# Optimization experiments

Measured on AMD Instinct MI355X. Metric: run time of the kernel, lower is better.

## Reference

```python
import jax, jax.numpy as jnp
import numpy as np
from jax import lax

D_MODEL = 64
D_STATE = 16
D_CONV = 3
EXPAND = 2
D_INNER = EXPAND * D_MODEL  # 128
DT_RANK = (D_MODEL + 15) // 16  # 4
B, H, W = 2, 64, 64


def setup_inputs() -> dict:
    key = jax.random.key(0)
    ks = jax.random.split(key, 8)
    def n(k, shape, s=0.02):
        return jax.random.normal(k, shape, dtype=jnp.float32) * s
    return {
        "x": jax.random.normal(ks[0], (B, D_MODEL, H, W), dtype=jnp.float32),
        "ln_w": jnp.ones((D_MODEL,), jnp.float32),
        "ln_b": jnp.zeros((D_MODEL,), jnp.float32),
        "W_in": n(ks[1], (4, 2 * D_INNER, D_MODEL)),          # in_proj per direction
        "conv_w": n(ks[2], (4, D_INNER, 1, D_CONV), 0.1),     # depthwise causal conv
        "conv_b": jnp.zeros((4, D_INNER), jnp.float32),
        "W_xproj": n(ks[3], (4, DT_RANK + 2 * D_STATE, D_INNER)),
        "W_dt": n(ks[4], (4, D_INNER, DT_RANK), 0.1),
        "b_dt": n(ks[5], (4, D_INNER), 0.1),
        "A_log": jnp.log(jnp.broadcast_to(jnp.arange(1, D_STATE + 1, dtype=jnp.float32), (4, D_INNER, D_STATE))),
        "D_param": jnp.ones((4, D_INNER), jnp.float32),
        "W_out": n(ks[6], (4, D_MODEL, D_INNER)),
    }


def _mamba(x, W_in, conv_w, conv_b, W_xproj, W_dt, b_dt, A_log, Dp, W_out):
    # x: (B, L, D) -> (B, L, D). Standard Mamba forward with selective scan.
    xz = x @ W_in.T                              # (B, L, 2*d_inner)
    xp, z = jnp.split(xz, 2, axis=-1)
    xc = jnp.swapaxes(xp, 1, 2)                  # (B, d_inner, L)
    xc = lax.conv_general_dilated(xc, conv_w, (1,), [(D_CONV - 1, 0)], feature_group_count=D_INNER)
    xc = xc + conv_b[None, :, None]
    xp = jax.nn.silu(jnp.swapaxes(xc, 1, 2))     # (B, L, d_inner)
    dbl = xp @ W_xproj.T                         # (B, L, dt_rank + 2*d_state)
    dt = dbl[..., :DT_RANK]
    Bc = dbl[..., DT_RANK:DT_RANK + D_STATE]
    Cc = dbl[..., DT_RANK + D_STATE:]
    dt = jax.nn.softplus(dt @ W_dt.T + b_dt)     # (B, L, d_inner)
    A = -jnp.exp(A_log)                          # (d_inner, d_state)
    dA = jnp.exp(dt[..., None] * A)              # (B, L, d_inner, d_state)
    dBu = (dt * xp)[..., None] * Bc[:, :, None, :]

    def comb(c1, c2):
        a1, b1 = c1
        a2, b2 = c2
        return a1 * a2, a2 * b1 + b2

    _, h = lax.associative_scan(comb, (dA, dBu), axis=1)  # parallel linear recurrence
    y = jnp.einsum('blds,bls->bld', h, Cc) + xp * Dp
    y = y * jax.nn.silu(z)
    return y @ W_out.T


def reference(x, ln_w, ln_b, W_in, conv_w, conv_b, W_xproj, W_dt, b_dt, A_log, D_param, W_out):
    Bq, C, Hh, Ww = x.shape
    xn = jnp.transpose(x, (0, 2, 3, 1))          # (B, H, W, C)
    mu = xn.mean(-1, keepdims=True)
    var = xn.var(-1, keepdims=True)
    xn = (xn - mu) * lax.rsqrt(var + 1e-5) * ln_w + ln_b
    x_f = xn.reshape(Bq, Hh * Ww, C)                              # row-major scan
    x_tf = jnp.transpose(xn, (0, 2, 1, 3)).reshape(Bq, Ww * Hh, C)  # column-major scan
    xs = jnp.stack([x_f, x_f[:, ::-1], x_tf, x_tf[:, ::-1]])      # (4, B, L, C)
    ys = jax.vmap(_mamba)(xs, W_in, conv_w, conv_b, W_xproj, W_dt, b_dt, A_log, D_param, W_out)
    y = ys[0].reshape(Bq, Hh, Ww, C) + ys[1][:, ::-1].reshape(Bq, Hh, Ww, C)
    yt = ys[2].reshape(Bq, Ww, Hh, C) + ys[3][:, ::-1].reshape(Bq, Ww, Hh, C)
    y = y + jnp.transpose(yt, (0, 2, 1, 3))
    return jnp.transpose(y, (0, 3, 1, 2))        # back to (B, C, H, W)
```

## Files before the change

kernel.cpp:

```cpp
#include <hip/hip_runtime.h>
#include <math.h>


#define PP  8
#define LL  4096
#define DD  128
#define CH  16
#define NCH 256
#define LOG2E 1.4426950408889634f
#define EXP2F(x) __builtin_exp2f(x)

__device__ __forceinline__ float sigmoidf_(float x){ return 1.0f/(1.0f+__expf(-x)); }

__device__ __forceinline__ int dirmap(int dir, int t) {
  if (dir == 0) return t;
  if (dir == 1) return 4095 - t;
  int tt = (dir == 2) ? t : 4095 - t;
  return ((tt & 63) << 6) | (tt >> 6);
}

__global__ __launch_bounds__(256) void k_ln(const float* __restrict__ x,
    const float* __restrict__ lw, const float* __restrict__ lb, float* __restrict__ xn) {
  int tid = threadIdx.x;
  int lane = tid & 63;
  int pos = blockIdx.x*4 + (tid>>6);
  int b = pos >> 12, hw = pos & 4095;
  float v = x[((long)(b*64 + lane))*4096 + hw];
  float s = v;
  for (int m = 32; m; m >>= 1) s += __shfl_xor(s, m);
  float mu = s * (1.0f/64.0f);
  float dv = (v-mu)*(v-mu);
  for (int m = 32; m; m >>= 1) dv += __shfl_xor(dv, m);
  float rs = rsqrtf(dv*(1.0f/64.0f) + 1e-5f);
  xn[(long)pos*64 + lane] = (v-mu)*rs*lw[lane] + lb[lane];
}

__global__ __launch_bounds__(256) void k_gemm1(const float* __restrict__ xn,
    const float* __restrict__ Win, float* __restrict__ xz) {
  __shared__ float Ast[64][68];
  __shared__ float Bst[64][68];
  int p = blockIdx.z, dir = p >> 1, b = p & 1;
  int tid = threadIdx.x;
  int tx = tid & 15, ty = tid >> 4;
  int m0 = blockIdx.x*64, n0 = blockIdx.y*64;
  int kk4 = tid & 15, rr = tid >> 4;
  #pragma unroll
  for (int pass = 0; pass < 4; ++pass) {
    int r = pass*16 + rr;
    int l = dirmap(dir, m0 + r);
    float4 av = *(const float4*)(xn + ((long)(b*4096 + l))*64 + kk4*4);
    Ast[kk4*4+0][r]=av.x; Ast[kk4*4+1][r]=av.y; Ast[kk4*4+2][r]=av.z; Ast[kk4*4+3][r]=av.w;
    float4 bv = *(const float4*)(Win + ((long)(dir*256 + n0 + r))*64 + kk4*4);
    Bst[kk4*4+0][r]=bv.x; Bst[kk4*4+1][r]=bv.y; Bst[kk4*4+2][r]=bv.z; Bst[kk4*4+3][r]=bv.w;
  }
  __syncthreads();
  float acc[4][4] = {};
  #pragma unroll 8
  for (int kk = 0; kk < 64; ++kk) {
    float4 a = *(const float4*)(&Ast[kk][ty*4]);
    float4 bq = *(const float4*)(&Bst[kk][tx*4]);
    acc[0][0] += a.x*bq.x; acc[0][1] += a.x*bq.y; acc[0][2] += a.x*bq.z; acc[0][3] += a.x*bq.w;
    acc[1][0] += a.y*bq.x; acc[1][1] += a.y*bq.y; acc[1][2] += a.y*bq.z; acc[1][3] += a.y*bq.w;
    acc[2][0] += a.z*bq.x; acc[2][1] += a.z*bq.y; acc[2][2] += a.z*bq.z; acc[2][3] += a.z*bq.w;
    acc[3][0] += a.w*bq.x; acc[3][1] += a.w*bq.y; acc[3][2] += a.w*bq.z; acc[3][3] += a.w*bq.w;
  }
  float* Cp = xz + (long)p*4096*256;
  #pragma unroll
  for (int i = 0; i < 4; ++i)
    #pragma unroll
    for (int j = 0; j < 4; ++j)
      Cp[(long)(m0 + ty*4 + i)*256 + n0 + tx*4 + j] = acc[i][j];
}

__global__ __launch_bounds__(256) void k_gemm(const float* __restrict__ A, const float* __restrict__ Bw,
    float* __restrict__ C, int M, int N, int K, long aStr, long bStr, long cStr) {
  __shared__ float Ast[64][68];
  __shared__ float Bst[64][68];
  int pair = blockIdx.z;
  const float* Ap = A + (long)pair*aStr;
  const float* Bp = Bw + (long)(pair>>1)*bStr;
  float* Cp = C + (long)pair*cStr;
  int tid = threadIdx.x;
  int tx = tid & 15, ty = tid >> 4;
  int m0 = blockIdx.x*64, n0 = blockIdx.y*64;
  int kk4 = tid & 15, rr = tid >> 4;
  float acc[4][4] = {};
  for (int ko = 0; ko < K; ko += 64) {
    for (int pass = 0; pass < 4; ++pass) {
      int r = pass*16 + rr;
      float4 av = *(const float4*)(Ap + (long)(m0+r)*K + ko + kk4*4);
      Ast[kk4*4+0][r]=av.x; Ast[kk4*4+1][r]=av.y; Ast[kk4*4+2][r]=av.z; Ast[kk4*4+3][r]=av.w;
      int j = n0 + r;
      float4 bv = make_float4(0.f,0.f,0.f,0.f);
      if (j < N) bv = *(const float4*)(Bp + (long)j*K + ko + kk4*4);
      Bst[kk4*4+0][r]=bv.x; Bst[kk4*4+1][r]=bv.y; Bst[kk4*4+2][r]=bv.z; Bst[kk4*4+3][r]=bv.w;
    }
    __syncthreads();
    #pragma unroll 8
    for (int kk = 0; kk < 64; ++kk) {
      float4 a = *(const float4*)(&Ast[kk][ty*4]);
      float4 b = *(const float4*)(&Bst[kk][tx*4]);
      acc[0][0] += a.x*b.x; acc[0][1] += a.x*b.y; acc[0][2] += a.x*b.z; acc[0][3] += a.x*b.w;
      acc[1][0] += a.y*b.x; acc[1][1] += a.y*b.y; acc[1][2] += a.y*b.z; acc[1][3] += a.y*b.w;
      acc[2][0] += a.z*b.x; acc[2][1] += a.z*b.y; acc[2][2] += a.z*b.z; acc[2][3] += a.z*b.w;
      acc[3][0] += a.w*b.x; acc[3][1] += a.w*b.y; acc[3][2] += a.w*b.z; acc[3][3] += a.w*b.w;
    }
    __syncthreads();
  }
  for (int i = 0; i < 4; ++i)
    for (int j = 0; j < 4; ++j) {
      int m = m0 + ty*4 + i, n = n0 + tx*4 + j;
      if (n < N) Cp[(long)m*N + n] = acc[i][j];
    }
}

__global__ __launch_bounds__(256) void k_conv(const float* __restrict__ xz, const float* __restrict__ cw,
    const float* __restrict__ cb, float* __restrict__ u) {
  int gid = blockIdx.x*256 + threadIdx.x;
  int d = gid & 127;
  int t = (gid >> 7) & 4095;
  int p = gid >> 19;
  int dir = p >> 1;
  const float* base = xz + ((long)p*4096)*256 + d;
  float x2 = base[(long)t*256];
  float x1 = (t >= 1) ? base[(long)(t-1)*256] : 0.f;
  float x0 = (t >= 2) ? base[(long)(t-2)*256] : 0.f;
  const float* w = cw + (dir*128 + d)*3;
  float a = x0*w[0] + x1*w[1] + x2*w[2] + cb[dir*128 + d];
  u[gid] = a * sigmoidf_(a);
}

__global__ __launch_bounds__(256) void k_dt(const float* __restrict__ dbl, const float* __restrict__ wdt,
    const float* __restrict__ bdt, float* __restrict__ dt) {
  int gid = blockIdx.x*256 + threadIdx.x;
  int d = gid & 127;
  int t = (gid >> 7) & 4095;
  int p = gid >> 19;
  int dir = p >> 1;
  const float* r = dbl + ((long)p*4096 + t)*36;
  float4 w = *(const float4*)(wdt + ((dir*128 + d) << 2));
  float lin = r[0]*w.x + r[1]*w.y + r[2]*w.z + r[3]*w.w + bdt[dir*128 + d];
  float sp = (lin > 20.f) ? lin : log1pf(__expf(lin));
  dt[gid] = sp;
}

__global__ __launch_bounds__(128) void k_scan1(const float* __restrict__ dt, const float* __restrict__ u,
    const float* __restrict__ dbl, const float* __restrict__ alog,
    float* __restrict__ pend, float* __restrict__ dAc) {
  int ch = blockIdx.x, p = blockIdx.y, dir = p >> 1;
  int d = threadIdx.x;
  __shared__ float Bsm[CH*16];
  long rowbase = (long)p*LL + ch*CH;
  #pragma unroll
  for (int k = 0; k < 2; ++k) {
    int idx = d + k*128;
    Bsm[idx] = dbl[(rowbase + (idx >> 4))*36 + 4 + (idx & 15)];
  }
  float A2[16], ps[16];
  const float* ab = alog + ((dir*DD + d) << 4);
  #pragma unroll
  for (int s = 0; s < 16; ++s) { A2[s] = -__expf(ab[s])*LOG2E; ps[s] = 0.f; }
  float sd = 0.f;
  __syncthreads();
  float dtn = dt[rowbase*DD + d];
  float un  = u [rowbase*DD + d];
  #pragma unroll 2
  for (int t = 0; t < CH; ++t) {
    float dtv = dtn, uv = un;
    if (t + 1 < CH) {
      dtn = dt[(rowbase + t + 1)*DD + d];
      un  = u [(rowbase + t + 1)*DD + d];
    }
    float dtu = dtv*uv;
    sd += dtv;
    const float* Bs = &Bsm[t*16];
    #pragma unroll
    for (int s = 0; s < 16; ++s) {
      float dA = EXP2F(dtv*A2[s]);
      ps[s] = fmaf(dA, ps[s], dtu*Bs[s]);
    }
  }
  long base = ((long)(p*NCH + ch)*DD + d)*16;
  #pragma unroll
  for (int s = 0; s < 16; ++s) {
    pend[base+s] = ps[s];
    dAc [base+s] = EXP2F(A2[s]*sd);
  }
}

__global__ __launch_bounds__(256) void k_scan2(const float* __restrict__ pend,
    const float* __restrict__ dAc, float* __restrict__ carry) {
  int g = blockIdx.x*256 + threadIdx.x;
  long hi = ((long)(g >> 11)) * ((long)NCH*2048);
  int lo = g & 2047;
  float a0[8], p0[8], a1[8], p1[8];
  #pragma unroll
  for (int i = 0; i < 8; ++i) {
    long ix = hi + (long)i*2048 + lo;
    a0[i] = dAc[ix]; p0[i] = pend[ix];
  }
  float c = 0.f;
  for (int chk = 0; chk < NCH; chk += 16) {
    #pragma unroll
    for (int i = 0; i < 8; ++i) {
      long ix = hi + (long)(chk + 8 + i)*2048 + lo;
      a1[i] = dAc[ix]; p1[i] = pend[ix];
    }
    #pragma unroll
    for (int i = 0; i < 8; ++i) {
      long ix = hi + (long)(chk + i)*2048 + lo;
      carry[ix] = c; c = fmaf(a0[i], c, p0[i]);
    }
    if (chk + 16 < NCH) {
      #pragma unroll
      for (int i = 0; i < 8; ++i) {
        long ix = hi + (long)(chk + 16 + i)*2048 + lo;
        a0[i] = dAc[ix]; p0[i] = pend[ix];
      }
    }
    #pragma unroll
    for (int i = 0; i < 8; ++i) {
      long ix = hi + (long)(chk + 8 + i)*2048 + lo;
      carry[ix] = c; c = fmaf(a1[i], c, p1[i]);
    }
  }
}

__global__ __launch_bounds__(128) void k_scan3(const float* __restrict__ dt, const float* __restrict__ u,
    const float* __restrict__ dbl, const float* __restrict__ xz, const float* __restrict__ alog,
    const float* __restrict__ Dp, const float* __restrict__ carry, float* __restrict__ y) {
  int ch = blockIdx.x, p = blockIdx.y, dir = p >> 1;
  int d = threadIdx.x;
  __shared__ float Bsm[CH*16];
  __shared__ float Csm[CH*16];
  long rowbase = (long)p*LL + ch*CH;
  #pragma unroll
  for (int k = 0; k < 4; ++k) {
    int idx = d + k*128;
    int half = idx >> 8;
    int e = idx & 255;
    float v = dbl[(rowbase + (e >> 4))*36 + (half ? 20 : 4) + (e & 15)];
    if (half) Csm[e] = v; else Bsm[e] = v;
  }
  float A2[16], h[16];
  const float* ab = alog + ((dir*DD + d) << 4);
  long cbase = ((long)(p*NCH + ch)*DD + d)*16;
  #pragma unroll
  for (int s = 0; s < 16; ++s) {
    A2[s] = -__expf(ab[s])*LOG2E;
    h[s] = carry[cbase + s];
  }
  float Dv = Dp[dir*DD + d];
  __syncthreads();
  float dtn = dt[rowbase*DD + d];
  float un  = u [rowbase*DD + d];
  float zn  = xz[rowbase*256 + 128 + d];
  #pragma unroll 2
  for (int t = 0; t < CH; ++t) {
    float dtv = dtn, uv = un, zv = zn;
    if (t + 1 < CH) {
      dtn = dt[(rowbase + t + 1)*DD + d];
      un  = u [(rowbase + t + 1)*DD + d];
      zn  = xz[(rowbase + t + 1)*256 + 128 + d];
    }
    float dtu = dtv*uv;
    const float* Bs = &Bsm[t*16];
    const float* Cs = &Csm[t*16];
    float acc = 0.f;
    #pragma unroll
    for (int s = 0; s < 16; ++s) {
      float dA = EXP2F(dtv*A2[s]);
      h[s] = fmaf(dA, h[s], dtu*Bs[s]);
      acc = fmaf(h[s], Cs[s], acc);
    }
    float yv = acc + uv*Dv;
    yv *= zv * sigmoidf_(zv);
    y[(rowbase + t)*DD + d] = yv;
  }
}

__global__ __launch_bounds__(256) void k_comb(const float* __restrict__ yg, float* __restrict__ out) {
  __shared__ float ysm[64][65];
  int bh = blockIdx.x;
  int b = bh >> 6, h = bh & 63;
  int tid = threadIdx.x;
  int c = tid & 63, q = tid >> 6;
  #pragma unroll
  for (int i = 0; i < 16; ++i) {
    int w = q*16 + i;
    int t0 = (h << 6) | w;
    int t2 = (w << 6) | h;
    float v = yg[((long)(b*4096) + t0)*64 + c]
            + yg[((long)((2+b)*4096) + (4095 - t0))*64 + c]
            + yg[((long)((4+b)*4096) + t2)*64 + c]
            + yg[((long)((6+b)*4096) + (4095 - t2))*64 + c];
    ysm[w][c] = v;
  }
  __syncthreads();
  int w2 = tid & 63;
  #pragma unroll
  for (int i = 0; i < 16; ++i) {
    int cc = q*16 + i;
    out[((long)(b*64 + cc))*4096 + (h << 6) + w2] = ysm[w2][cc];
  }
}

extern "C" void kernel_launch(void* const* d_in, const int* in_sizes, int n_in,
                              void* d_out, int out_size, void* d_ws, size_t ws_size,
                              hipStream_t stream) {
  const float* x      = (const float*)d_in[0];
  const float* ln_w   = (const float*)d_in[1];
  const float* ln_b   = (const float*)d_in[2];
  const float* W_in   = (const float*)d_in[3];
  const float* conv_w = (const float*)d_in[4];
  const float* conv_b = (const float*)d_in[5];
  const float* W_xp   = (const float*)d_in[6];
  const float* W_dt   = (const float*)d_in[7];
  const float* b_dt   = (const float*)d_in[8];
  const float* A_log  = (const float*)d_in[9];
  const float* D_par  = (const float*)d_in[10];
  const float* W_out  = (const float*)d_in[11];

  float* ws    = (float*)d_ws;
  float* xn    = ws;
  float* xz    = xn    + 524288;
  float* u     = xz    + 8388608;
  float* dblb  = u     + 4194304;
  float* dtb   = dblb  + 1179648;
  float* pend  = dtb   + 4194304;
  float* dAc   = pend  + 4194304;
  float* carry = dAc   + 4194304;
  float* ybuf  = carry + 4194304;
  float* yg    = ybuf  + 4194304;

  k_ln   <<<2048, 256, 0, stream>>>(x, ln_w, ln_b, xn);
  k_gemm1<<<dim3(64,4,8), 256, 0, stream>>>(xn, W_in, xz);
  k_conv <<<16384, 256, 0, stream>>>(xz, conv_w, conv_b, u);
  k_gemm <<<dim3(64,1,8), 256, 0, stream>>>(u, W_xp, dblb, 4096, 36, 128,
                                            4096L*128, 36L*128, 4096L*36);
  k_dt   <<<16384, 256, 0, stream>>>(dblb, W_dt, b_dt, dtb);
  k_scan1<<<dim3(NCH,PP), 128, 0, stream>>>(dtb, u, dblb, A_log, pend, dAc);
  k_scan2<<<64, 256, 0, stream>>>(pend, dAc, carry);
  k_scan3<<<dim3(NCH,PP), 128, 0, stream>>>(dtb, u, dblb, xz, A_log, D_par, carry, ybuf);
  k_gemm <<<dim3(64,1,8), 256, 0, stream>>>(ybuf, W_out, yg, 4096, 64, 128,
                                            4096L*128, 64L*128, 4096L*64);
  k_comb <<<128, 256, 0, stream>>>(yg, (float*)d_out);
}
```

Measured before the change: 239.3 us.

## Fuse conv into in-proj GEMM, dt into x-proj, out-proj into scan; double chunk size

The depthwise conv and SiLU move into the in-projection GEMM epilogue, using a 2-row halo so the xz intermediate is never written. The dt projection and softplus are folded into the x-projection kernel, and the output projection runs inside scan3 from shared memory, which removes the ybuf round trip. The scan chunk grows from 16 to 32, halving the chunk-state buffers and reshaping scan2 to 256 blocks of 64 threads. Together this cuts four launches and several large global intermediates, at the cost of more shared memory per block, about 3% extra GEMM work for the halo, and half as many scan blocks.

```diff
diff --git a/kernel.cpp b/kernel.cpp
--- a/kernel.cpp
+++ b/kernel.cpp
@@ -5,8 +5,8 @@
 #define PP  8
 #define LL  4096
 #define DD  128
-#define CH  16
-#define NCH 256
+#define CH  32
+#define NCH 128
 #define LOG2E 1.4426950408889634f
 #define EXP2F(x) __builtin_exp2f(x)
 
@@ -35,8 +35,9 @@
   xn[(long)pos*64 + lane] = (v-mu)*rs*lw[lane] + lb[lane];
 }
 
-__global__ __launch_bounds__(256) void k_gemm1(const float* __restrict__ xn,
-    const float* __restrict__ Win, float* __restrict__ xz) {
+__global__ __launch_bounds__(256) void k_front(const float* __restrict__ xn,
+    const float* __restrict__ Win, const float* __restrict__ cw, const float* __restrict__ cb,
+    float* __restrict__ u, float* __restrict__ zb) {
   __shared__ float Ast[64][68];
   __shared__ float Bst[64][68];
   int p = blockIdx.z, dir = p >> 1, b = p & 1;
@@ -45,54 +46,90 @@
   int m0 = blockIdx.x*64, n0 = blockIdx.y*64;
   int kk4 = tid & 15, rr = tid >> 4;
   #pragma unroll
-  for (int pass = 0; pass < 4; ++pass) {
+  for (int pass = 0; pass < 5; ++pass) {
     int r = pass*16 + rr;
-    int l = dirmap(dir, m0 + r);
-    float4 av = *(const float4*)(xn + ((long)(b*4096 + l))*64 + kk4*4);
-    Ast[kk4*4+0][r]=av.x; Ast[kk4*4+1][r]=av.y; Ast[kk4*4+2][r]=av.z; Ast[kk4*4+3][r]=av.w;
-    float4 bv = *(const float4*)(Win + ((long)(dir*256 + n0 + r))*64 + kk4*4);
-    Bst[kk4*4+0][r]=bv.x; Bst[kk4*4+1][r]=bv.y; Bst[kk4*4+2][r]=bv.z; Bst[kk4*4+3][r]=bv.w;
-  }
-  __syncthreads();
-  float acc[4][4] = {};
-  #pragma unroll 8
+    if (r < 66) {
+      int gl = m0 - 2 + r;
+      float4 av = make_float4(0.f,0.f,0.f,0.f);
+      if (gl >= 0 && gl < 4096) {
+        int l = dirmap(dir, gl);
+        av = *(const float4*)(xn + ((long)(b*4096 + l))*64 + kk4*4);
+      }
+      Ast[kk4*4+0][r]=av.x; Ast[kk4*4+1][r]=av.y; Ast[kk4*4+2][r]=av.z; Ast[kk4*4+3][r]=av.w;
+    }
+    if (r < 64) {
+      float4 bv = *(const float4*)(Win + ((long)(dir*256 + n0 + r))*64 + kk4*4);
+      Bst[kk4*4+0][r]=bv.x; Bst[kk4*4+1][r]=bv.y; Bst[kk4*4+2][r]=bv.z; Bst[kk4*4+3][r]=bv.w;
+    }
+  }
+  __syncthreads();
+  float acc[6][4] = {};
+  #pragma unroll 4
   for (int kk = 0; kk < 64; ++kk) {
-    float4 a = *(const float4*)(&Ast[kk][ty*4]);
-    float4 bq = *(const float4*)(&Bst[kk][tx*4]);
-    acc[0][0] += a.x*bq.x; acc[0][1] += a.x*bq.y; acc[0][2] += a.x*bq.z; acc[0][3] += a.x*bq.w;
-    acc[1][0] += a.y*bq.x; acc[1][1] += a.y*bq.y; acc[1][2] += a.y*bq.z; acc[1][3] += a.y*bq.w;
-    acc[2][0] += a.z*bq.x; acc[2][1] += a.z*bq.y; acc[2][2] += a.z*bq.z; acc[2][3] += a.z*bq.w;
-    acc[3][0] += a.w*bq.x; acc[3][1] += a.w*bq.y; acc[3][2] += a.w*bq.z; acc[3][3] += a.w*bq.w;
-  }
-  float* Cp = xz + (long)p*4096*256;
-  #pragma unroll
-  for (int i = 0; i < 4; ++i)
-    #pragma unroll
-    for (int j = 0; j < 4; ++j)
-      Cp[(long)(m0 + ty*4 + i)*256 + n0 + tx*4 + j] = acc[i][j];
-}
-
-__global__ __launch_bounds__(256) void k_gemm(const float* __restrict__ A, const float* __restrict__ Bw,
-    float* __restrict__ C, int M, int N, int K, long aStr, long bStr, long cStr) {
+    float4 a4 = *(const float4*)(&Ast[kk][ty*4]);
+    float2 a2 = *(const float2*)(&Ast[kk][ty*4+4]);
+    float4 b4 = *(const float4*)(&Bst[kk][tx*4]);
+    float av[6] = {a4.x,a4.y,a4.z,a4.w,a2.x,a2.y};
+    float bv[4] = {b4.x,b4.y,b4.z,b4.w};
+    #pragma unroll
+    for (int i = 0; i < 6; ++i)
+      #pragma unroll
+      for (int j = 0; j < 4; ++j)
+        acc[i][j] = fmaf(av[i], bv[j], acc[i][j]);
+  }
+  if (n0 < 128) {
+    float w0[4], w1[4], w2[4], bb[4];
+    #pragma unroll
+    for (int jj = 0; jj < 4; ++jj) {
+      int n = n0 + tx*4 + jj;
+      const float* w = cw + (dir*128 + n)*3;
+      w0[jj]=w[0]; w1[jj]=w[1]; w2[jj]=w[2]; bb[jj]=cb[dir*128 + n];
+    }
+    #pragma unroll
+    for (int j = 0; j < 4; ++j) {
+      int t = m0 + ty*4 + j;
+      float vals[4];
+      #pragma unroll
+      for (int jj = 0; jj < 4; ++jj) {
+        float a = fmaf(acc[j][jj], w0[jj], fmaf(acc[j+1][jj], w1[jj],
+                  fmaf(acc[j+2][jj], w2[jj], bb[jj])));
+        vals[jj] = a * sigmoidf_(a);
+      }
+      *(float4*)(u + ((long)p*LL + t)*DD + n0 + tx*4) =
+        make_float4(vals[0],vals[1],vals[2],vals[3]);
+    }
+  } else {
+    #pragma unroll
+    for (int j = 0; j < 4; ++j) {
+      int t = m0 + ty*4 + j;
+      *(float4*)(zb + ((long)p*LL + t)*DD + (n0-128) + tx*4) =
+        make_float4(acc[j+2][0],acc[j+2][1],acc[j+2][2],acc[j+2][3]);
+    }
+  }
+}
+
+__global__ __launch_bounds__(256) void k_xprojdt(const float* __restrict__ u,
+    const float* __restrict__ Wxp, const float* __restrict__ wdt, const float* __restrict__ bdt,
+    float* __restrict__ dbl, float* __restrict__ dt) {
   __shared__ float Ast[64][68];
   __shared__ float Bst[64][68];
-  int pair = blockIdx.z;
-  const float* Ap = A + (long)pair*aStr;
-  const float* Bp = Bw + (long)(pair>>1)*bStr;
-  float* Cp = C + (long)pair*cStr;
+  __shared__ float Csm[64][5];
+  int p = blockIdx.z, dir = p >> 1;
+  const float* Ap = u + (long)p*LL*DD;
+  const float* Bp = Wxp + (long)dir*36*DD;
   int tid = threadIdx.x;
   int tx = tid & 15, ty = tid >> 4;
-  int m0 = blockIdx.x*64, n0 = blockIdx.y*64;
+  int m0 = blockIdx.x*64;
   int kk4 = tid & 15, rr = tid >> 4;
   float acc[4][4] = {};
-  for (int ko = 0; ko < K; ko += 64) {
+  for (int ko = 0; ko < 128; ko += 64) {
+    #pragma unroll
     for (int pass = 0; pass < 4; ++pass) {
       int r = pass*16 + rr;
-      float4 av = *(const float4*)(Ap + (long)(m0+r)*K + ko + kk4*4);
+      float4 av = *(const float4*)(Ap + (long)(m0+r)*DD + ko + kk4*4);
       Ast[kk4*4+0][r]=av.x; Ast[kk4*4+1][r]=av.y; Ast[kk4*4+2][r]=av.z; Ast[kk4*4+3][r]=av.w;
-      int j = n0 + r;
       float4 bv = make_float4(0.f,0.f,0.f,0.f);
-      if (j < N) bv = *(const float4*)(Bp + (long)j*K + ko + kk4*4);
+      if (r < 36) bv = *(const float4*)(Bp + (long)r*DD + ko + kk4*4);
       Bst[kk4*4+0][r]=bv.x; Bst[kk4*4+1][r]=bv.y; Bst[kk4*4+2][r]=bv.z; Bst[kk4*4+3][r]=bv.w;
     }
     __syncthreads();
@@ -107,41 +144,33 @@
     }
     __syncthreads();
   }
+  float* Cp = dbl + (long)p*LL*36;
+  #pragma unroll
   for (int i = 0; i < 4; ++i)
+    #pragma unroll
     for (int j = 0; j < 4; ++j) {
-      int m = m0 + ty*4 + i, n = n0 + tx*4 + j;
-      if (n < N) Cp[(long)m*N + n] = acc[i][j];
-    }
-}
-
-__global__ __launch_bounds__(256) void k_conv(const float* __restrict__ xz, const float* __restrict__ cw,
-    const float* __restrict__ cb, float* __restrict__ u) {
-  int gid = blockIdx.x*256 + threadIdx.x;
-  int d = gid & 127;
-  int t = (gid >> 7) & 4095;
-  int p = gid >> 19;
-  int dir = p >> 1;
-  const float* base = xz + ((long)p*4096)*256 + d;
-  float x2 = base[(long)t*256];
-  float x1 = (t >= 1) ? base[(long)(t-1)*256] : 0.f;
-  float x0 = (t >= 2) ? base[(long)(t-2)*256] : 0.f;
-  const float* w = cw + (dir*128 + d)*3;
-  float a = x0*w[0] + x1*w[1] + x2*w[2] + cb[dir*128 + d];
-  u[gid] = a * sigmoidf_(a);
-}
-
-__global__ __launch_bounds__(256) void k_dt(const float* __restrict__ dbl, const float* __restrict__ wdt,
-    const float* __restrict__ bdt, float* __restrict__ dt) {
-  int gid = blockIdx.x*256 + threadIdx.x;
-  int d = gid & 127;
-  int t = (gid >> 7) & 4095;
-  int p = gid >> 19;
-  int dir = p >> 1;
-  const float* r = dbl + ((long)p*4096 + t)*36;
-  float4 w = *(const float4*)(wdt + ((dir*128 + d) << 2));
-  float lin = r[0]*w.x + r[1]*w.y + r[2]*w.z + r[3]*w.w + bdt[dir*128 + d];
-  float sp = (lin > 20.f) ? lin : log1pf(__expf(lin));
-  dt[gid] = sp;
+      int n = tx*4 + j;
+      if (n < 36) Cp[(long)(m0 + ty*4 + i)*36 + n] = acc[i][j];
+    }
+  if (tx == 0) {
+    #pragma unroll
+    for (int i = 0; i < 4; ++i)
+      #pragma unroll
+      for (int j = 0; j < 4; ++j)
+        Csm[ty*4+i][j] = acc[i][j];
+  }
+  __syncthreads();
+  int d = tid & 127;
+  float4 wv = *(const float4*)(wdt + ((dir*DD + d) << 2));
+  float bv = bdt[dir*DD + d];
+  #pragma unroll 4
+  for (int it = 0; it < 32; ++it) {
+    int t = 2*it + (tid >> 7);
+    float lin = fmaf(Csm[t][0], wv.x, fmaf(Csm[t][1], wv.y,
+                fmaf(Csm[t][2], wv.z, fmaf(Csm[t][3], wv.w, bv))));
+    float sp = (lin > 20.f) ? lin : __logf(1.f + __expf(lin));
+    dt[((long)p*LL + m0 + t)*DD + d] = sp;
+  }
 }
 
 __global__ __launch_bounds__(128) void k_scan1(const float* __restrict__ dt, const float* __restrict__ u,
@@ -152,7 +181,7 @@
   __shared__ float Bsm[CH*16];
   long rowbase = (long)p*LL + ch*CH;
   #pragma unroll
-  for (int k = 0; k < 2; ++k) {
+  for (int k = 0; k < 4; ++k) {
     int idx = d + k*128;
     Bsm[idx] = dbl[(rowbase + (idx >> 4))*36 + 4 + (idx & 15)];
   }
@@ -188,9 +217,9 @@
   }
 }
 
-__global__ __launch_bounds__(256) void k_scan2(const float* __restrict__ pend,
+__global__ __launch_bounds__(64) void k_scan2(const float* __restrict__ pend,
     const float* __restrict__ dAc, float* __restrict__ carry) {
-  int g = blockIdx.x*256 + threadIdx.x;
+  int g = blockIdx.x*64 + threadIdx.x;
   long hi = ((long)(g >> 11)) * ((long)NCH*2048);
   int lo = g & 2047;
   float a0[8], p0[8], a1[8], p1[8];
@@ -227,20 +256,33 @@
 }
 
 __global__ __launch_bounds__(128) void k_scan3(const float* __restrict__ dt, const float* __restrict__ u,
-    const float* __restrict__ dbl, const float* __restrict__ xz, const float* __restrict__ alog,
-    const float* __restrict__ Dp, const float* __restrict__ carry, float* __restrict__ y) {
+    const float* __restrict__ dbl, const float* __restrict__ zb, const float* __restrict__ alog,
+    const float* __restrict__ Dp, const float* __restrict__ carry,
+    const float* __restrict__ Wout, float* __restrict__ yg) {
   int ch = blockIdx.x, p = blockIdx.y, dir = p >> 1;
   int d = threadIdx.x;
   __shared__ float Bsm[CH*16];
   __shared__ float Csm[CH*16];
+  __shared__ float ysm[128][36];
+  __shared__ float Wsm[128][66];
   long rowbase = (long)p*LL + ch*CH;
   #pragma unroll
-  for (int k = 0; k < 4; ++k) {
+  for (int k = 0; k < 8; ++k) {
     int idx = d + k*128;
-    int half = idx >> 8;
-    int e = idx & 255;
+    int half = idx >> 9;
+    int e = idx & 511;
     float v = dbl[(rowbase + (e >> 4))*36 + (half ? 20 : 4) + (e & 15)];
     if (half) Csm[e] = v; else Bsm[e] = v;
+  }
+  {
+    const float* Wo = Wout + (long)dir*64*DD;
+    #pragma unroll
+    for (int q = 0; q < 16; ++q) {
+      int f = d + 128*q;
+      int c = f >> 5, k4 = f & 31;
+      float4 w4 = *(const float4*)(Wo + c*DD + k4*4);
+      Wsm[k4*4+0][c]=w4.x; Wsm[k4*4+1][c]=w4.y; Wsm[k4*4+2][c]=w4.z; Wsm[k4*4+3][c]=w4.w;
+    }
   }
   float A2[16], h[16];
   const float* ab = alog + ((dir*DD + d) << 4);
@@ -254,14 +296,14 @@
   __syncthreads();
   float dtn = dt[rowbase*DD + d];
   float un  = u [rowbase*DD + d];
-  float zn  = xz[rowbase*256 + 128 + d];
+  float zn  = zb[rowbase*DD + d];
   #pragma unroll 2
   for (int t = 0; t < CH; ++t) {
     float dtv = dtn, uv = un, zv = zn;
     if (t + 1 < CH) {
       dtn = dt[(rowbase + t + 1)*DD + d];
       un  = u [(rowbase + t + 1)*DD + d];
-      zn  = xz[(rowbase + t + 1)*256 + 128 + d];
+      zn  = zb[(rowbase + t + 1)*DD + d];
     }
     float dtu = dtv*uv;
     const float* Bs = &Bsm[t*16];
@@ -275,8 +317,28 @@
     }
     float yv = acc + uv*Dv;
     yv *= zv * sigmoidf_(zv);
-    y[(rowbase + t)*DD + d] = yv;
-  }
+    ysm[d][t] = yv;
+  }
+  __syncthreads();
+  int ry = d >> 4;
+  int cx = d & 15;
+  float ag[4][4] = {};
+  #pragma unroll 4
+  for (int k = 0; k < 128; ++k) {
+    float4 y4 = *(const float4*)(&ysm[k][ry*4]);
+    float4 w4 = *(const float4*)(&Wsm[k][cx*4]);
+    float yv[4] = {y4.x,y4.y,y4.z,y4.w};
+    float wv[4] = {w4.x,w4.y,w4.z,w4.w};
+    #pragma unroll
+    for (int i = 0; i < 4; ++i)
+      #pragma unroll
+      for (int j = 0; j < 4; ++j)
+        ag[i][j] = fmaf(yv[i], wv[j], ag[i][j]);
+  }
+  #pragma unroll
+  for (int i = 0; i < 4; ++i)
+    *(float4*)(yg + ((long)p*LL + ch*CH + ry*4 + i)*64 + cx*4) =
+      make_float4(ag[i][0],ag[i][1],ag[i][2],ag[i][3]);
 }
 
 __global__ __launch_bounds__(256) void k_comb(const float* __restrict__ yg, float* __restrict__ out) {
@@ -323,26 +385,21 @@
 
   float* ws    = (float*)d_ws;
   float* xn    = ws;
-  float* xz    = xn    + 524288;
-  float* u     = xz    + 8388608;
-  float* dblb  = u     + 4194304;
+  float* u     = xn    + 524288;
+  float* zb    = u     + 4194304;
+  float* dblb  = zb    + 4194304;
   float* dtb   = dblb  + 1179648;
   float* pend  = dtb   + 4194304;
-  float* dAc   = pend  + 4194304;
-  float* carry = dAc   + 4194304;
-  float* ybuf  = carry + 4194304;
-  float* yg    = ybuf  + 4194304;
-
-  k_ln   <<<2048, 256, 0, stream>>>(x, ln_w, ln_b, xn);
-  k_gemm1<<<dim3(64,4,8), 256, 0, stream>>>(xn, W_in, xz);
-  k_conv <<<16384, 256, 0, stream>>>(xz, conv_w, conv_b, u);
-  k_gemm <<<dim3(64,1,8), 256, 0, stream>>>(u, W_xp, dblb, 4096, 36, 128,
-                                            4096L*128, 36L*128, 4096L*36);
-  k_dt   <<<16384, 256, 0, stream>>>(dblb, W_dt, b_dt, dtb);
-  k_scan1<<<dim3(NCH,PP), 128, 0, stream>>>(dtb, u, dblb, A_log, pend, dAc);
-  k_scan2<<<64, 256, 0, stream>>>(pend, dAc, carry);
-  k_scan3<<<dim3(NCH,PP), 128, 0, stream>>>(dtb, u, dblb, xz, A_log, D_par, carry, ybuf);
-  k_gemm <<<dim3(64,1,8), 256, 0, stream>>>(ybuf, W_out, yg, 4096, 64, 128,
-                                            4096L*128, 64L*128, 4096L*64);
-  k_comb <<<128, 256, 0, stream>>>(yg, (float*)d_out);
-}
+  float* dAc   = pend  + 2097152;
+  float* carry = dAc   + 2097152;
+  float* yg    = carry + 2097152;
+
+  k_ln     <<<2048, 256, 0, stream>>>(x, ln_w, ln_b, xn);
+  k_front  <<<dim3(64,4,PP), 256, 0, stream>>>(xn, W_in, conv_w, conv_b, u, zb);
+  k_xprojdt<<<dim3(64,1,PP), 256, 0, stream>>>(u, W_xp, W_dt, b_dt, dblb, dtb);
+  k_scan1  <<<dim3(NCH,PP), 128, 0, stream>>>(dtb, u, dblb, A_log, pend, dAc);
+  k_scan2  <<<256, 64, 0, stream>>>(pend, dAc, carry);
+  k_scan3  <<<dim3(NCH,PP), 128, 0, stream>>>(dtb, u, dblb, zb, A_log, D_par, carry,
+                                              W_out, yg);
+  k_comb   <<<128, 256, 0, stream>>>(yg, (float*)d_out);
+}
```

After: 230.0 us. 1.04x faster.
